# Performance work log

Measured on AMD Instinct MI355X. Metric: run time of the kernel, lower is better.

The kernel has to match this reference:

```python
import jax, jax.numpy as jnp
import numpy as np

B, L, C, NH = 4, 2048, 512, 8
HD = C // NH  # head_dim = 64


def setup_inputs() -> dict:
    key = jax.random.key(0)
    k1, k2, k3, k4 = jax.random.split(key, 4)
    s = 1.0 / np.sqrt(C)
    return {
        "x": jax.random.normal(k1, (B, L, C), dtype=jnp.float32),
        "w_qkv": jax.random.normal(k2, (C, 3 * C), dtype=jnp.float32) * s,
        "b_qkv": jnp.zeros((3 * C,), dtype=jnp.float32),  # zeroed in __init__
        "w_proj": jax.random.normal(k3, (C, C), dtype=jnp.float32) * s,
        "b_proj": jax.random.normal(k4, (C,), dtype=jnp.float32) * 0.01,
    }


def reference(x, w_qkv, b_qkv, w_proj, b_proj):
    Bx, Lx, Cx = x.shape
    qkv = x @ w_qkv + b_qkv                       # [B, L, 3C]
    qkv = qkv.reshape(Bx, Lx, 3, NH, HD)          # 'B L (K H D)'
    qkv = jnp.transpose(qkv, (2, 0, 3, 1, 4))     # 'K B H L D'
    q, k, v = qkv[0], qkv[1], qkv[2]
    scale = 1.0 / np.sqrt(HD)
    scores = jnp.einsum('bhld,bhmd->bhlm', q, k) * scale  # [B, H, L, L]
    attn = jax.nn.softmax(scores, axis=-1)
    out = jnp.einsum('bhlm,bhmd->bhld', attn, v)  # [B, H, L, D]
    out = jnp.transpose(out, (0, 2, 1, 3)).reshape(Bx, Lx, Cx)  # 'B H L D -> B L (H D)'
    return out @ w_proj + b_proj
```

## Files before the change

### kernel.cpp

```cpp
#include <hip/hip_runtime.h>

#define B_   4
#define L_   2048
#define C_   512
#define NH_  8
#define HD_  64
#define M_   (B_ * L_)
#define N_QKV 1536

typedef __bf16 bf16x8 __attribute__((ext_vector_type(8)));
typedef float floatx4 __attribute__((ext_vector_type(4)));
typedef unsigned short ushort_t;

__device__ __forceinline__ unsigned pk2(float a, float b) {
  union { float f; unsigned u; } x, y;
  x.f = a; y.f = b;
  return __builtin_amdgcn_perm(y.u + 0x8000u, x.u + 0x8000u, 0x07060302u);
}

__device__ __forceinline__ ushort_t bf16h(float a) {
  union { float f; unsigned u; } x;
  x.f = a;
  return (ushort_t)((x.u + 0x8000u) >> 16);
}

__device__ __forceinline__ floatx4 mfma16(bf16x8 a, bf16x8 b, floatx4 c) {
  return __builtin_amdgcn_mfma_f32_16x16x32_bf16(a, b, c, 0, 0, 0);
}

__device__ __forceinline__ void gld_lds16(const void* g, void* s) {
  __builtin_amdgcn_global_load_lds(
      (const __attribute__((address_space(1))) unsigned int*)(g),
      (__attribute__((address_space(3))) unsigned int*)(s), 16, 0, 0);
}

__global__ __launch_bounds__(256) void convert_all_kernel(
    const float* __restrict__ x, const float* __restrict__ wq,
    const float* __restrict__ wp, ushort_t* __restrict__ xb,
    ushort_t* __restrict__ wqT, ushort_t* __restrict__ wpT) {
  __shared__ ushort_t tile[64][68];
  const int t = threadIdx.x;
  const int bid = blockIdx.x;
  if (bid < 2048) {
    size_t i = ((size_t)bid * 256 + t) * 8;
    float4 a = *(const float4*)(x + i);
    float4 b = *(const float4*)(x + i + 4);
    uint4 o;
    o.x = pk2(a.x, a.y);
    o.y = pk2(a.z, a.w);
    o.z = pk2(b.x, b.y);
    o.w = pk2(b.z, b.w);
    *(uint4*)(xb + i) = o;
    return;
  }
  const float* w;
  ushort_t* wt;
  int N, n0, k0;
  if (bid < 2240) {
    int b2 = bid - 2048;
    w = wq; wt = wqT; N = N_QKV;
    n0 = (b2 % 24) * 64; k0 = (b2 / 24) * 64;
  } else {
    int b2 = bid - 2240;
    w = wp; wt = wpT; N = C_;
    n0 = (b2 & 7) * 64; k0 = (b2 >> 3) * 64;
  }
  const int r = t >> 4, c4 = (t & 15) * 4;
#pragma unroll
  for (int i = 0; i < 4; ++i) {
    int k = r + i * 16;
    float4 v = *(const float4*)(w + (size_t)(k0 + k) * N + n0 + c4);
    uint2 p;
    p.x = pk2(v.x, v.y);
    p.y = pk2(v.z, v.w);
    *(uint2*)&tile[k][c4] = p;
  }
  __syncthreads();
#pragma unroll
  for (int i = 0; i < 4; ++i) {
    int n = r + i * 16;
    uint2 o;
    o.x = (unsigned)tile[c4 + 0][n] | ((unsigned)tile[c4 + 1][n] << 16);
    o.y = (unsigned)tile[c4 + 2][n] | ((unsigned)tile[c4 + 3][n] << 16);
    *(uint2*)(wt + (size_t)(n0 + n) * 512 + k0 + c4) = o;
  }
}

__global__ __launch_bounds__(256) void qkv_mfma_kernel(
    const ushort_t* __restrict__ A,
    const ushort_t* __restrict__ Bt,
    const float* __restrict__ bias,
    ushort_t* __restrict__ Qd, ushort_t* __restrict__ Kd,
    ushort_t* __restrict__ Vd) {
  __shared__ ushort_t As[2][4096];
  __shared__ ushort_t Bs[2][2048];

  const int t = threadIdx.x;
  const int w = t >> 6, l = t & 63;
  const int li = l & 15, lq = l >> 4;
  const int m0 = blockIdx.x * 128;
  const int n0 = blockIdx.y * 64;

  const int inner = (l & 7) ^ (l >> 3);
  const int srow = (l >> 3) * 2 + (inner >> 2);
  const int skb = inner & 3;

  const ushort_t* asrc0 = A + (size_t)(m0 + (2 * w) * 16 + srow) * 512 + skb * 8;
  const ushort_t* asrc1 = A + (size_t)(m0 + (2 * w + 1) * 16 + srow) * 512 + skb * 8;
  const ushort_t* bsrc0 = Bt + (size_t)(n0 + w * 16 + srow) * 512 + skb * 8;
  const int qo0 = (2 * w) * 512, qo1 = (2 * w + 1) * 512;
  const int bo0 = w * 512;

  const int foff = (li >> 1) * 128 + ((((li & 1) * 4 + lq)) ^ (li >> 1)) * 16;

  const floatx4 fz = {0.f, 0.f, 0.f, 0.f};
  floatx4 acc[2][4];
#pragma unroll
  for (int i = 0; i < 2; ++i)
#pragma unroll
    for (int j = 0; j < 4; ++j) acc[i][j] = fz;

  for (int kk = 0; kk < 8; ++kk) {
    __syncthreads();
#pragma unroll
    for (int kh = 0; kh < 2; ++kh) {
      gld_lds16(asrc0 + kh * 32, &As[kh][qo0]);
      gld_lds16(asrc1 + kh * 32, &As[kh][qo1]);
      gld_lds16(bsrc0 + kh * 32, &Bs[kh][bo0]);
    }
    asrc0 += 64; asrc1 += 64; bsrc0 += 64;
    __syncthreads();

#pragma unroll
    for (int kh = 0; kh < 2; ++kh) {
      bf16x8 af[2], bfr[4];
#pragma unroll
      for (int mt = 0; mt < 2; ++mt)
        af[mt] = *(const bf16x8*)((const char*)&As[kh][0] +
                                  (w * 32 + mt * 16) * 64 + foff);
#pragma unroll
      for (int nt = 0; nt < 4; ++nt)
        bfr[nt] = *(const bf16x8*)((const char*)&Bs[kh][0] +
                                   (nt * 16) * 64 + foff);
#pragma unroll
      for (int mt = 0; mt < 2; ++mt)
#pragma unroll
        for (int nt = 0; nt < 4; ++nt)
          acc[mt][nt] = mfma16(af[mt], bfr[nt], acc[mt][nt]);
    }
  }

  const int kk2 = n0 >> 9, h = (n0 >> 6) & 7;
  const int mb = m0 + w * 32;
  const int b = m0 >> 11;
  const int bh = b * NH_ + h;
  const float SCQ = 0.18033688011f;
  float bb[4];
#pragma unroll
  for (int nt = 0; nt < 4; ++nt) bb[nt] = bias[n0 + nt * 16 + li];

  if (kk2 == 0) {
#pragma unroll
    for (int mt = 0; mt < 2; ++mt) {
      int lrow = (mb + mt * 16 + lq * 4) & (L_ - 1);
#pragma unroll
      for (int nt = 0; nt < 4; ++nt) {
        int d = nt * 16 + li;
        ushort_t* p = Qd + ((size_t)bh * L_ + lrow) * HD_ + d;
#pragma unroll
        for (int r = 0; r < 4; ++r)
          p[(size_t)r * HD_] = bf16h((acc[mt][nt][r] + bb[nt]) * SCQ);
      }
    }
  } else if (kk2 == 1) {
#pragma unroll
    for (int mt = 0; mt < 2; ++mt) {
      int lrow = (mb + mt * 16 + lq * 4) & (L_ - 1);
#pragma unroll
      for (int nt = 0; nt < 4; ++nt) {
        int d = nt * 16 + li;
        ushort_t* p = Kd + ((size_t)bh * L_ + lrow) * HD_ + d;
#pragma unroll
        for (int r = 0; r < 4; ++r)
          p[(size_t)r * HD_] = bf16h(acc[mt][nt][r] + bb[nt]);
      }
    }
  } else {
#pragma unroll
    for (int mt = 0; mt < 2; ++mt) {
      int tb = mb + mt * 16 + lq * 4;
      int key = tb & 63;
      int c = (tb >> 6) & 31;
      int sp = key >> 5;
      int rem = key & 31;
      int lq2 = rem >> 3;
      int h8 = (rem >> 2) & 1;
#pragma unroll
      for (int nt = 0; nt < 4; ++nt) {
        size_t off = ((size_t)(bh * 32 + c) * 512 +
                      ((sp * 4 + nt) * 4 + lq2) * 16 + li) * 8 + h8 * 4;
        uint2 v;
        v.x = pk2(acc[mt][nt][0] + bb[nt], acc[mt][nt][1] + bb[nt]);
        v.y = pk2(acc[mt][nt][2] + bb[nt], acc[mt][nt][3] + bb[nt]);
        *(uint2*)(Vd + off) = v;
      }
    }
  }
}

__global__ __launch_bounds__(512) void attn_kernel(
    const ushort_t* __restrict__ Qg, const ushort_t* __restrict__ Kg,
    const ushort_t* __restrict__ Vb, ushort_t* __restrict__ AO) {
  __shared__ __align__(16) char smem[35328];
  ushort_t* KsB = (ushort_t*)smem;
  ushort_t* VsB = (ushort_t*)(smem + 16384);
  float* Oc = (float*)smem;
  float* Lc = (float*)(smem + 34816);

  const int t = threadIdx.x;
  const int w = t >> 6, l = t & 63;
  const int g2 = w >> 2, wl = w & 3;
  const int li = l & 15, lq = l >> 4;
  const int bh = blockIdx.x & 31;
  const int m0 = (blockIdx.x >> 5) * 128;

  ushort_t* Ks = KsB + g2 * 4096;
  ushort_t* Vs = VsB + g2 * 4096;

  const ushort_t* ksrc[2];
  const ushort_t* vsrc[2];
  int koff[2];
#pragma unroll
  for (int u = 0; u < 2; ++u) {
    int p = (2 * wl + u) * 64 + l;
    int key = p >> 3, pb = p & 7;
    int swz = (key & 3) | (((key >> 3) & 1) << 2);
    ksrc[u] = Kg + ((size_t)bh * L_ + g2 * 1024 + key) * HD_ + (pb ^ swz) * 8;
    vsrc[u] = Vb + ((size_t)bh * 32 * 512 + (size_t)g2 * 16 * 512 + p) * 8;
    koff[u] = p * 8;
  }

  bf16x8 qf[2][2];
#pragma unroll
  for (int g = 0; g < 2; ++g)
#pragma unroll
    for (int s = 0; s < 2; ++s)
      qf[g][s] = *(const bf16x8*)(Qg +
          ((size_t)bh * L_ + m0 + wl * 32 + 16 * g + li) * HD_ + 32 * s + lq * 8);

  const floatx4 fz = {0.f, 0.f, 0.f, 0.f};
  floatx4 O[2][4];
  float lsum[2] = {0.f, 0.f};
#pragma unroll
  for (int g = 0; g < 2; ++g)
#pragma unroll
    for (int dt = 0; dt < 4; ++dt) O[g][dt] = fz;

  const int keybase = 8 * (li >> 2) + (li & 3);
  const int xsw = li & 7;

  for (int c = 0; c < 16; ++c) {
    __syncthreads();
#pragma unroll
    for (int u = 0; u < 2; ++u) {
      gld_lds16(ksrc[u], Ks + koff[u]);
      gld_lds16(vsrc[u], Vs + koff[u]);
      ksrc[u] += 64 * HD_;
      vsrc[u] += 4096;
    }
    __syncthreads();

#pragma unroll
    for (int sp = 0; sp < 2; ++sp) {
      floatx4 sa[2][2];
#pragma unroll
      for (int g = 0; g < 2; ++g)
#pragma unroll
        for (int k2 = 0; k2 < 2; ++k2) sa[g][k2] = fz;

#pragma unroll
      for (int k2 = 0; k2 < 2; ++k2) {
        const char* rowb =
            (const char*)Ks + (32 * sp + 4 * k2 + keybase) * 128;
#pragma unroll
        for (int s = 0; s < 2; ++s) {
          bf16x8 kf = *(const bf16x8*)(rowb + ((4 * s + lq) ^ xsw) * 16);
          sa[0][k2] = mfma16(kf, qf[0][s], sa[0][k2]);
          sa[1][k2] = mfma16(kf, qf[1][s], sa[1][k2]);
        }
      }

      bf16x8 pf[2];
#pragma unroll
      for (int g = 0; g < 2; ++g) {
        float pv[2][4];
#pragma unroll
        for (int k2 = 0; k2 < 2; ++k2)
#pragma unroll
          for (int r = 0; r < 4; ++r) {
            float e = __builtin_amdgcn_exp2f(sa[g][k2][r]);
            pv[k2][r] = e;
            lsum[g] += e;
          }
        uint4 pk;
        pk.x = pk2(pv[0][0], pv[0][1]);
        pk.y = pk2(pv[0][2], pv[0][3]);
        pk.z = pk2(pv[1][0], pv[1][1]);
        pk.w = pk2(pv[1][2], pv[1][3]);
        pf[g] = __builtin_bit_cast(bf16x8, pk);
      }

#pragma unroll
      for (int dt = 0; dt < 4; ++dt) {
        bf16x8 vf = *(const bf16x8*)((const char*)Vs +
            sp * 4096 + dt * 1024 + lq * 256 + li * 16);
        O[0][dt] = mfma16(vf, pf[0], O[0][dt]);
        O[1][dt] = mfma16(vf, pf[1], O[1][dt]);
      }
    }
  }

  float srow[2];
#pragma unroll
  for (int g = 0; g < 2; ++g) {
    float s = lsum[g];
    s += __shfl_xor(s, 16, 64);
    s += __shfl_xor(s, 32, 64);
    srow[g] = s;
  }

  __syncthreads();
  if (g2 == 1) {
#pragma unroll
    for (int g = 0; g < 2; ++g) {
      int row = wl * 32 + 16 * g + li;
#pragma unroll
      for (int dt = 0; dt < 4; ++dt)
        *(floatx4*)&Oc[row * 68 + 16 * dt + 4 * lq] = O[g][dt];
      Lc[row] = srow[g];
    }
  }
  __syncthreads();

  if (g2 == 0) {
    const int b = bh >> 3, h = bh & 7;
#pragma unroll
    for (int g = 0; g < 2; ++g) {
      int row = wl * 32 + 16 * g + li;
      float inv = 1.0f / (srow[g] + Lc[row]);
      int qrow = m0 + row;
      ushort_t* base = AO + ((size_t)(b * L_ + qrow)) * C_ + h * HD_ + 4 * lq;
#pragma unroll
      for (int dt = 0; dt < 4; ++dt) {
        floatx4 oc = *(const floatx4*)&Oc[row * 68 + 16 * dt + 4 * lq];
        floatx4 ot = O[g][dt] + oc;
        uint2 v;
        v.x = pk2(ot[0] * inv, ot[1] * inv);
        v.y = pk2(ot[2] * inv, ot[3] * inv);
        *(uint2*)(base + 16 * dt) = v;
      }
    }
  }
}

__global__ __launch_bounds__(256) void proj_mfma_kernel(
    const ushort_t* __restrict__ A,
    const ushort_t* __restrict__ Bt,
    const float* __restrict__ bias, float* __restrict__ out) {
  __shared__ ushort_t As[2][2048];
  __shared__ ushort_t Bs[2][2048];

  const int t = threadIdx.x;
  const int w = t >> 6, l = t & 63;
  const int li = l & 15, lq = l >> 4;
  const int m0 = blockIdx.x * 64;
  const int n0 = blockIdx.y * 64;

  const int inner = (l & 7) ^ (l >> 3);
  const int srow = (l >> 3) * 2 + (inner >> 2);
  const int skb = inner & 3;

  const ushort_t* asrc0 = A + (size_t)(m0 + w * 16 + srow) * 512 + skb * 8;
  const ushort_t* bsrc0 = Bt + (size_t)(n0 + w * 16 + srow) * 512 + skb * 8;
  const int qo0 = w * 512;

  const int foff = (li >> 1) * 128 + ((((li & 1) * 4 + lq)) ^ (li >> 1)) * 16;

  const floatx4 fz = {0.f, 0.f, 0.f, 0.f};
  floatx4 acc[4];
#pragma unroll
  for (int j = 0; j < 4; ++j) acc[j] = fz;

  for (int kk = 0; kk < 8; ++kk) {
    __syncthreads();
#pragma unroll
    for (int kh = 0; kh < 2; ++kh) {
      gld_lds16(asrc0 + kh * 32, &As[kh][qo0]);
      gld_lds16(bsrc0 + kh * 32, &Bs[kh][qo0]);
    }
    asrc0 += 64; bsrc0 += 64;
    __syncthreads();

#pragma unroll
    for (int kh = 0; kh < 2; ++kh) {
      bf16x8 af, bfr[4];
      af = *(const bf16x8*)((const char*)&As[kh][0] + (w * 16) * 64 + foff);
#pragma unroll
      for (int nt = 0; nt < 4; ++nt)
        bfr[nt] = *(const bf16x8*)((const char*)&Bs[kh][0] +
                                   (nt * 16) * 64 + foff);
#pragma unroll
      for (int nt = 0; nt < 4; ++nt)
        acc[nt] = mfma16(af, bfr[nt], acc[nt]);
    }
  }

  const int m = m0 + w * 16 + lq * 4;
#pragma unroll
  for (int nt = 0; nt < 4; ++nt) {
    int n = n0 + nt * 16 + li;
    float bb = bias[n];
#pragma unroll
    for (int r = 0; r < 4; ++r)
      out[(size_t)(m + r) * C_ + n] = acc[nt][r] + bb;
  }
}

extern "C" void kernel_launch(void* const* d_in, const int* in_sizes, int n_in,
                              void* d_out, int out_size, void* d_ws,
                              size_t ws_size, hipStream_t stream) {
  const float* x      = (const float*)d_in[0];
  const float* w_qkv  = (const float*)d_in[1];
  const float* b_qkv  = (const float*)d_in[2];
  const float* w_proj = (const float*)d_in[3];
  const float* b_proj = (const float*)d_in[4];
  float* out = (float*)d_out;

  ushort_t* ws     = (ushort_t*)d_ws;
  ushort_t* Qd     = ws;
  ushort_t* Kd     = ws + 4194304;
  ushort_t* Vd     = ws + 8388608;
  ushort_t* AO     = ws + 12582912;
  ushort_t* xb     = ws + 16777216;
  ushort_t* wqkvT  = ws + 20971520;
  ushort_t* wprojT = ws + 21757952;

  convert_all_kernel<<<2304, 256, 0, stream>>>(x, w_qkv, w_proj, xb, wqkvT,
                                               wprojT);

  dim3 g1(M_ / 128, N_QKV / 64);
  qkv_mfma_kernel<<<g1, 256, 0, stream>>>(xb, wqkvT, b_qkv, Qd, Kd, Vd);

  attn_kernel<<<512, 512, 0, stream>>>(Qd, Kd, Vd, AO);

  dim3 g3(M_ / 64, C_ / 64);
  proj_mfma_kernel<<<g3, 256, 0, stream>>>(AO, wprojT, b_proj, out);
}
```

Baseline: 148.5 us.

## Enlarge QKV GEMM tile to 128x128 and remap blocks per XCD

The QKV GEMM block tile grows from 128x64 to 128x128, with a 2x2 wave layout in which each wave computes a 64x64 sub-tile. This raises operand reuse from shared memory and halves the number of blocks. Both GEMMs now launch on a 1D grid whose block index is remapped so each XCD gets a contiguous band of M rows, aiming for better L2 locality of shared A/B tiles. The larger tile doubles accumulator registers and LDS use, which may lower occupancy. The V scatter index math is also rewritten to match the new per-wave row layout.

```diff
diff --git a/kernel.cpp b/kernel.cpp
--- a/kernel.cpp
+++ b/kernel.cpp
@@ -93,13 +93,16 @@
     ushort_t* __restrict__ Qd, ushort_t* __restrict__ Kd,
     ushort_t* __restrict__ Vd) {
   __shared__ ushort_t As[2][4096];
-  __shared__ ushort_t Bs[2][2048];
+  __shared__ ushort_t Bs[2][4096];
 
   const int t = threadIdx.x;
   const int w = t >> 6, l = t & 63;
   const int li = l & 15, lq = l >> 4;
-  const int m0 = blockIdx.x * 128;
-  const int n0 = blockIdx.y * 64;
+  const int wm = w & 1, wn = w >> 1;
+  const int bid = blockIdx.x;
+  const int xcd = bid & 7, idx = bid >> 3;
+  const int m0 = (xcd * 8 + idx / 12) * 128;
+  const int n0 = (idx % 12) * 128;
 
   const int inner = (l & 7) ^ (l >> 3);
   const int srow = (l >> 3) * 2 + (inner >> 2);
@@ -107,16 +110,16 @@
 
   const ushort_t* asrc0 = A + (size_t)(m0 + (2 * w) * 16 + srow) * 512 + skb * 8;
   const ushort_t* asrc1 = A + (size_t)(m0 + (2 * w + 1) * 16 + srow) * 512 + skb * 8;
-  const ushort_t* bsrc0 = Bt + (size_t)(n0 + w * 16 + srow) * 512 + skb * 8;
+  const ushort_t* bsrc0 = Bt + (size_t)(n0 + (2 * w) * 16 + srow) * 512 + skb * 8;
+  const ushort_t* bsrc1 = Bt + (size_t)(n0 + (2 * w + 1) * 16 + srow) * 512 + skb * 8;
   const int qo0 = (2 * w) * 512, qo1 = (2 * w + 1) * 512;
-  const int bo0 = w * 512;
 
   const int foff = (li >> 1) * 128 + ((((li & 1) * 4 + lq)) ^ (li >> 1)) * 16;
 
   const floatx4 fz = {0.f, 0.f, 0.f, 0.f};
-  floatx4 acc[2][4];
-#pragma unroll
-  for (int i = 0; i < 2; ++i)
+  floatx4 acc[4][4];
+#pragma unroll
+  for (int i = 0; i < 4; ++i)
 #pragma unroll
     for (int j = 0; j < 4; ++j) acc[i][j] = fz;
 
@@ -126,42 +129,44 @@
     for (int kh = 0; kh < 2; ++kh) {
       gld_lds16(asrc0 + kh * 32, &As[kh][qo0]);
       gld_lds16(asrc1 + kh * 32, &As[kh][qo1]);
-      gld_lds16(bsrc0 + kh * 32, &Bs[kh][bo0]);
-    }
-    asrc0 += 64; asrc1 += 64; bsrc0 += 64;
+      gld_lds16(bsrc0 + kh * 32, &Bs[kh][qo0]);
+      gld_lds16(bsrc1 + kh * 32, &Bs[kh][qo1]);
+    }
+    asrc0 += 64; asrc1 += 64; bsrc0 += 64; bsrc1 += 64;
     __syncthreads();
 
 #pragma unroll
     for (int kh = 0; kh < 2; ++kh) {
-      bf16x8 af[2], bfr[4];
-#pragma unroll
-      for (int mt = 0; mt < 2; ++mt)
+      bf16x8 af[4], bfr[4];
+#pragma unroll
+      for (int mt = 0; mt < 4; ++mt)
         af[mt] = *(const bf16x8*)((const char*)&As[kh][0] +
-                                  (w * 32 + mt * 16) * 64 + foff);
+                                  (wm * 64 + mt * 16) * 64 + foff);
 #pragma unroll
       for (int nt = 0; nt < 4; ++nt)
         bfr[nt] = *(const bf16x8*)((const char*)&Bs[kh][0] +
-                                   (nt * 16) * 64 + foff);
-#pragma unroll
-      for (int mt = 0; mt < 2; ++mt)
+                                   (wn * 64 + nt * 16) * 64 + foff);
+#pragma unroll
+      for (int mt = 0; mt < 4; ++mt)
 #pragma unroll
         for (int nt = 0; nt < 4; ++nt)
           acc[mt][nt] = mfma16(af[mt], bfr[nt], acc[mt][nt]);
     }
   }
 
-  const int kk2 = n0 >> 9, h = (n0 >> 6) & 7;
-  const int mb = m0 + w * 32;
-  const int b = m0 >> 11;
+  const int n0g = n0 + wn * 64;
+  const int kk2 = n0g >> 9, h = (n0g >> 6) & 7;
+  const int mb = m0 + wm * 64;
+  const int b = mb >> 11;
   const int bh = b * NH_ + h;
   const float SCQ = 0.18033688011f;
   float bb[4];
 #pragma unroll
-  for (int nt = 0; nt < 4; ++nt) bb[nt] = bias[n0 + nt * 16 + li];
+  for (int nt = 0; nt < 4; ++nt) bb[nt] = bias[n0g + nt * 16 + li];
 
   if (kk2 == 0) {
 #pragma unroll
-    for (int mt = 0; mt < 2; ++mt) {
+    for (int mt = 0; mt < 4; ++mt) {
       int lrow = (mb + mt * 16 + lq * 4) & (L_ - 1);
 #pragma unroll
       for (int nt = 0; nt < 4; ++nt) {
@@ -174,7 +179,7 @@
     }
   } else if (kk2 == 1) {
 #pragma unroll
-    for (int mt = 0; mt < 2; ++mt) {
+    for (int mt = 0; mt < 4; ++mt) {
       int lrow = (mb + mt * 16 + lq * 4) & (L_ - 1);
 #pragma unroll
       for (int nt = 0; nt < 4; ++nt) {
@@ -187,12 +192,11 @@
     }
   } else {
 #pragma unroll
-    for (int mt = 0; mt < 2; ++mt) {
+    for (int mt = 0; mt < 4; ++mt) {
       int tb = mb + mt * 16 + lq * 4;
-      int key = tb & 63;
       int c = (tb >> 6) & 31;
-      int sp = key >> 5;
-      int rem = key & 31;
+      int sp = (mt >> 1) & 1;
+      int rem = tb & 31;
       int lq2 = rem >> 3;
       int h8 = (rem >> 2) & 1;
 #pragma unroll
@@ -373,8 +377,10 @@
   const int t = threadIdx.x;
   const int w = t >> 6, l = t & 63;
   const int li = l & 15, lq = l >> 4;
-  const int m0 = blockIdx.x * 64;
-  const int n0 = blockIdx.y * 64;
+  const int bid = blockIdx.x;
+  const int xcd = bid & 7, idx = bid >> 3;
+  const int m0 = (xcd * 16 + (idx >> 3)) * 64;
+  const int n0 = (idx & 7) * 64;
 
   const int inner = (l & 7) ^ (l >> 3);
   const int srow = (l >> 3) * 2 + (inner >> 2);
@@ -448,11 +454,9 @@
   convert_all_kernel<<<2304, 256, 0, stream>>>(x, w_qkv, w_proj, xb, wqkvT,
                                                wprojT);
 
-  dim3 g1(M_ / 128, N_QKV / 64);
-  qkv_mfma_kernel<<<g1, 256, 0, stream>>>(xb, wqkvT, b_qkv, Qd, Kd, Vd);
+  qkv_mfma_kernel<<<768, 256, 0, stream>>>(xb, wqkvT, b_qkv, Qd, Kd, Vd);
 
   attn_kernel<<<512, 512, 0, stream>>>(Qd, Kd, Vd, AO);
 
-  dim3 g3(M_ / 64, C_ / 64);
-  proj_mfma_kernel<<<g3, 256, 0, stream>>>(AO, wprojT, b_proj, out);
-}
+  proj_mfma_kernel<<<1024, 256, 0, stream>>>(AO, wprojT, b_proj, out);
+}
```

After: 153.0 us. 3.0% more time.

## Split attention KV across four wave groups and remap GEMM blocks per XCD

Applied to the files above, without the earlier changes.

The attention kernel now handles 64 query rows per block with four wave-pairs, each covering a quarter of the keys. The partial outputs are merged through shared memory in three serialized steps, and the grid doubles to 1024 blocks. The QKV and projection GEMMs use a 1D grid remapped so that consecutive M tiles land on the same XCD, which should improve L2 reuse. In exchange, each block loads less per step and the serial reduction adds synchronization overhead.

```diff
diff --git a/kernel.cpp b/kernel.cpp
--- a/kernel.cpp
+++ b/kernel.cpp
@@ -98,8 +98,10 @@
   const int t = threadIdx.x;
   const int w = t >> 6, l = t & 63;
   const int li = l & 15, lq = l >> 4;
-  const int m0 = blockIdx.x * 128;
-  const int n0 = blockIdx.y * 64;
+  const int bid = blockIdx.x;
+  const int xcd = bid & 7, idx = bid >> 3;
+  const int m0 = (xcd * 8 + idx / 24) * 128;
+  const int n0 = (idx % 24) * 64;
 
   const int inner = (l & 7) ^ (l >> 3);
   const int srow = (l >> 3) * 2 + (inner >> 2);
@@ -208,35 +210,33 @@
   }
 }
 
-__global__ __launch_bounds__(512) void attn_kernel(
+__global__ __launch_bounds__(512, 8) void attn_kernel(
     const ushort_t* __restrict__ Qg, const ushort_t* __restrict__ Kg,
     const ushort_t* __restrict__ Vb, ushort_t* __restrict__ AO) {
-  __shared__ __align__(16) char smem[35328];
-  ushort_t* KsB = (ushort_t*)smem;
-  ushort_t* VsB = (ushort_t*)(smem + 16384);
-  float* Oc = (float*)smem;
-  float* Lc = (float*)(smem + 34816);
+  __shared__ __align__(16) char smem[32768];
 
   const int t = threadIdx.x;
   const int w = t >> 6, l = t & 63;
-  const int g2 = w >> 2, wl = w & 3;
+  const int g2 = w >> 1, wl = w & 1;
   const int li = l & 15, lq = l >> 4;
   const int bh = blockIdx.x & 31;
-  const int m0 = (blockIdx.x >> 5) * 128;
-
-  ushort_t* Ks = KsB + g2 * 4096;
-  ushort_t* Vs = VsB + g2 * 4096;
+  const int m0 = (blockIdx.x >> 5) * 64;
+
+  ushort_t* Ks = (ushort_t*)(smem + g2 * 4096);
+  ushort_t* Vs = (ushort_t*)(smem + 16384 + g2 * 4096);
+  float* Oc = (float*)smem;
+  float* Lc = (float*)(smem + 17408);
 
   const ushort_t* ksrc[2];
   const ushort_t* vsrc[2];
   int koff[2];
 #pragma unroll
   for (int u = 0; u < 2; ++u) {
-    int p = (2 * wl + u) * 64 + l;
+    int p = wl * 128 + u * 64 + l;
     int key = p >> 3, pb = p & 7;
     int swz = (key & 3) | (((key >> 3) & 1) << 2);
-    ksrc[u] = Kg + ((size_t)bh * L_ + g2 * 1024 + key) * HD_ + (pb ^ swz) * 8;
-    vsrc[u] = Vb + ((size_t)bh * 32 * 512 + (size_t)g2 * 16 * 512 + p) * 8;
+    ksrc[u] = Kg + ((size_t)bh * L_ + g2 * 512 + key) * HD_ + (pb ^ swz) * 8;
+    vsrc[u] = Vb + ((size_t)(bh * 32 + g2 * 8) * 512 + p) * 8;
     koff[u] = p * 8;
   }
 
@@ -265,58 +265,54 @@
     for (int u = 0; u < 2; ++u) {
       gld_lds16(ksrc[u], Ks + koff[u]);
       gld_lds16(vsrc[u], Vs + koff[u]);
-      ksrc[u] += 64 * HD_;
-      vsrc[u] += 4096;
-    }
-    __syncthreads();
-
-#pragma unroll
-    for (int sp = 0; sp < 2; ++sp) {
-      floatx4 sa[2][2];
-#pragma unroll
-      for (int g = 0; g < 2; ++g)
-#pragma unroll
-        for (int k2 = 0; k2 < 2; ++k2) sa[g][k2] = fz;
-
-#pragma unroll
-      for (int k2 = 0; k2 < 2; ++k2) {
-        const char* rowb =
-            (const char*)Ks + (32 * sp + 4 * k2 + keybase) * 128;
-#pragma unroll
-        for (int s = 0; s < 2; ++s) {
-          bf16x8 kf = *(const bf16x8*)(rowb + ((4 * s + lq) ^ xsw) * 16);
-          sa[0][k2] = mfma16(kf, qf[0][s], sa[0][k2]);
-          sa[1][k2] = mfma16(kf, qf[1][s], sa[1][k2]);
+      ksrc[u] += 32 * HD_;
+      vsrc[u] += 2048;
+    }
+    __syncthreads();
+
+    floatx4 sa[2][2];
+#pragma unroll
+    for (int g = 0; g < 2; ++g)
+#pragma unroll
+      for (int k2 = 0; k2 < 2; ++k2) sa[g][k2] = fz;
+
+#pragma unroll
+    for (int k2 = 0; k2 < 2; ++k2) {
+      const char* rowb = (const char*)Ks + (4 * k2 + keybase) * 128;
+#pragma unroll
+      for (int s = 0; s < 2; ++s) {
+        bf16x8 kf = *(const bf16x8*)(rowb + ((4 * s + lq) ^ xsw) * 16);
+        sa[0][k2] = mfma16(kf, qf[0][s], sa[0][k2]);
+        sa[1][k2] = mfma16(kf, qf[1][s], sa[1][k2]);
+      }
+    }
+
+    bf16x8 pf[2];
+#pragma unroll
+    for (int g = 0; g < 2; ++g) {
+      float pv[2][4];
+#pragma unroll
+      for (int k2 = 0; k2 < 2; ++k2)
+#pragma unroll
+        for (int r = 0; r < 4; ++r) {
+          float e = __builtin_amdgcn_exp2f(sa[g][k2][r]);
+          pv[k2][r] = e;
+          lsum[g] += e;
         }
-      }
-
-      bf16x8 pf[2];
-#pragma unroll
-      for (int g = 0; g < 2; ++g) {
-        float pv[2][4];
-#pragma unroll
-        for (int k2 = 0; k2 < 2; ++k2)
-#pragma unroll
-          for (int r = 0; r < 4; ++r) {
-            float e = __builtin_amdgcn_exp2f(sa[g][k2][r]);
-            pv[k2][r] = e;
-            lsum[g] += e;
-          }
-        uint4 pk;
-        pk.x = pk2(pv[0][0], pv[0][1]);
-        pk.y = pk2(pv[0][2], pv[0][3]);
-        pk.z = pk2(pv[1][0], pv[1][1]);
-        pk.w = pk2(pv[1][2], pv[1][3]);
-        pf[g] = __builtin_bit_cast(bf16x8, pk);
-      }
-
-#pragma unroll
-      for (int dt = 0; dt < 4; ++dt) {
-        bf16x8 vf = *(const bf16x8*)((const char*)Vs +
-            sp * 4096 + dt * 1024 + lq * 256 + li * 16);
-        O[0][dt] = mfma16(vf, pf[0], O[0][dt]);
-        O[1][dt] = mfma16(vf, pf[1], O[1][dt]);
-      }
+      uint4 pk;
+      pk.x = pk2(pv[0][0], pv[0][1]);
+      pk.y = pk2(pv[0][2], pv[0][3]);
+      pk.z = pk2(pv[1][0], pv[1][1]);
+      pk.w = pk2(pv[1][2], pv[1][3]);
+      pf[g] = __builtin_bit_cast(bf16x8, pk);
+    }
+
+#pragma unroll
+    for (int dt = 0; dt < 4; ++dt) {
+      bf16x8 vf = *(const bf16x8*)((const char*)Vs +
+          dt * 1024 + lq * 256 + li * 16);
+      O[0][dt] = mfma16(vf, pf[0], O[0][dt]);
+      O[1][dt] = mfma16(vf, pf[1], O[1][dt]);
     }
   }
 
@@ -330,18 +326,43 @@
   }
 
   __syncthreads();
-  if (g2 == 1) {
+  if (g2 == 3) {
 #pragma unroll
     for (int g = 0; g < 2; ++g) {
       int row = wl * 32 + 16 * g + li;
 #pragma unroll
       for (int dt = 0; dt < 4; ++dt)
         *(floatx4*)&Oc[row * 68 + 16 * dt + 4 * lq] = O[g][dt];
-      Lc[row] = srow[g];
+      if (lq == 0) Lc[row] = srow[g];
     }
   }
   __syncthreads();
-
+  if (g2 == 2) {
+#pragma unroll
+    for (int g = 0; g < 2; ++g) {
+      int row = wl * 32 + 16 * g + li;
+#pragma unroll
+      for (int dt = 0; dt < 4; ++dt) {
+        floatx4 oc = *(const floatx4*)&Oc[row * 68 + 16 * dt + 4 * lq];
+        *(floatx4*)&Oc[row * 68 + 16 * dt + 4 * lq] = oc + O[g][dt];
+      }
+      if (lq == 0) Lc[row] += srow[g];
+    }
+  }
+  __syncthreads();
+  if (g2 == 1) {
+#pragma unroll
+    for (int g = 0; g < 2; ++g) {
+      int row = wl * 32 + 16 * g + li;
+#pragma unroll
+      for (int dt = 0; dt < 4; ++dt) {
+        floatx4 oc = *(const floatx4*)&Oc[row * 68 + 16 * dt + 4 * lq];
+        *(floatx4*)&Oc[row * 68 + 16 * dt + 4 * lq] = oc + O[g][dt];
+      }
+      if (lq == 0) Lc[row] += srow[g];
+    }
+  }
+  __syncthreads();
   if (g2 == 0) {
     const int b = bh >> 3, h = bh & 7;
 #pragma unroll
@@ -373,8 +394,10 @@
   const int t = threadIdx.x;
   const int w = t >> 6, l = t & 63;
   const int li = l & 15, lq = l >> 4;
-  const int m0 = blockIdx.x * 64;
-  const int n0 = blockIdx.y * 64;
+  const int bid = blockIdx.x;
+  const int xcd = bid & 7, idx = bid >> 3;
+  const int m0 = (xcd * 16 + (idx >> 3)) * 64;
+  const int n0 = (idx & 7) * 64;
 
   const int inner = (l & 7) ^ (l >> 3);
   const int srow = (l >> 3) * 2 + (inner >> 2);
@@ -448,11 +471,9 @@
   convert_all_kernel<<<2304, 256, 0, stream>>>(x, w_qkv, w_proj, xb, wqkvT,
                                                wprojT);
 
-  dim3 g1(M_ / 128, N_QKV / 64);
-  qkv_mfma_kernel<<<g1, 256, 0, stream>>>(xb, wqkvT, b_qkv, Qd, Kd, Vd);
-
-  attn_kernel<<<512, 512, 0, stream>>>(Qd, Kd, Vd, AO);
-
-  dim3 g3(M_ / 64, C_ / 64);
-  proj_mfma_kernel<<<g3, 256, 0, stream>>>(AO, wprojT, b_proj, out);
-}
+  qkv_mfma_kernel<<<1536, 256, 0, stream>>>(xb, wqkvT, b_qkv, Qd, Kd, Vd);
+
+  attn_kernel<<<1024, 512, 0, stream>>>(Qd, Kd, Vd, AO);
+
+  proj_mfma_kernel<<<1024, 256, 0, stream>>>(AO, wprojT, b_proj, out);
+}
```

Result: slower. 335.5 us (+125.9%).

## Fuse x fp32-to-bf16 conversion into QKV GEMM tile loads

Applied to the files above, without the earlier changes.

Drops the standalone pass that converted x to bf16 and instead has the QKV GEMM load fp32 x directly, pack it to bf16 in registers and store it into shared memory. This removes one kernel launch and the write and re-read of a bf16 copy of x. In exchange, each GEMM column tile re-reads x at twice the byte width, and the A-tile load becomes a synchronous register round trip instead of an asynchronous direct-to-LDS load.

```diff
diff --git a/kernel.cpp b/kernel.cpp
--- a/kernel.cpp
+++ b/kernel.cpp
@@ -34,34 +34,20 @@
       (__attribute__((address_space(3))) unsigned int*)(s), 16, 0, 0);
 }
 
-__global__ __launch_bounds__(256) void convert_all_kernel(
-    const float* __restrict__ x, const float* __restrict__ wq,
-    const float* __restrict__ wp, ushort_t* __restrict__ xb,
+__global__ __launch_bounds__(256) void convert_w_kernel(
+    const float* __restrict__ wq, const float* __restrict__ wp,
     ushort_t* __restrict__ wqT, ushort_t* __restrict__ wpT) {
   __shared__ ushort_t tile[64][68];
   const int t = threadIdx.x;
   const int bid = blockIdx.x;
-  if (bid < 2048) {
-    size_t i = ((size_t)bid * 256 + t) * 8;
-    float4 a = *(const float4*)(x + i);
-    float4 b = *(const float4*)(x + i + 4);
-    uint4 o;
-    o.x = pk2(a.x, a.y);
-    o.y = pk2(a.z, a.w);
-    o.z = pk2(b.x, b.y);
-    o.w = pk2(b.z, b.w);
-    *(uint4*)(xb + i) = o;
-    return;
-  }
   const float* w;
   ushort_t* wt;
   int N, n0, k0;
-  if (bid < 2240) {
-    int b2 = bid - 2048;
+  if (bid < 192) {
     w = wq; wt = wqT; N = N_QKV;
-    n0 = (b2 % 24) * 64; k0 = (b2 / 24) * 64;
+    n0 = (bid % 24) * 64; k0 = (bid / 24) * 64;
   } else {
-    int b2 = bid - 2240;
+    int b2 = bid - 192;
     w = wp; wt = wpT; N = C_;
     n0 = (b2 & 7) * 64; k0 = (b2 >> 3) * 64;
   }
@@ -87,7 +73,7 @@
 }
 
 __global__ __launch_bounds__(256) void qkv_mfma_kernel(
-    const ushort_t* __restrict__ A,
+    const float* __restrict__ X,
     const ushort_t* __restrict__ Bt,
     const float* __restrict__ bias,
     ushort_t* __restrict__ Qd, ushort_t* __restrict__ Kd,
@@ -105,11 +91,12 @@
   const int srow = (l >> 3) * 2 + (inner >> 2);
   const int skb = inner & 3;
 
-  const ushort_t* asrc0 = A + (size_t)(m0 + (2 * w) * 16 + srow) * 512 + skb * 8;
-  const ushort_t* asrc1 = A + (size_t)(m0 + (2 * w + 1) * 16 + srow) * 512 + skb * 8;
+  const float* axsrc0 = X + (size_t)(m0 + (2 * w) * 16 + srow) * 512 + skb * 8;
+  const float* axsrc1 = X + (size_t)(m0 + (2 * w + 1) * 16 + srow) * 512 + skb * 8;
   const ushort_t* bsrc0 = Bt + (size_t)(n0 + w * 16 + srow) * 512 + skb * 8;
-  const int qo0 = (2 * w) * 512, qo1 = (2 * w + 1) * 512;
   const int bo0 = w * 512;
+  const int ao0 = (2 * w) * 512 + l * 8;
+  const int ao1 = (2 * w + 1) * 512 + l * 8;
 
   const int foff = (li >> 1) * 128 + ((((li & 1) * 4 + lq)) ^ (li >> 1)) * 16;
 
@@ -121,14 +108,31 @@
     for (int j = 0; j < 4; ++j) acc[i][j] = fz;
 
   for (int kk = 0; kk < 8; ++kk) {
-    __syncthreads();
-#pragma unroll
-    for (int kh = 0; kh < 2; ++kh) {
-      gld_lds16(asrc0 + kh * 32, &As[kh][qo0]);
-      gld_lds16(asrc1 + kh * 32, &As[kh][qo1]);
-      gld_lds16(bsrc0 + kh * 32, &Bs[kh][bo0]);
-    }
-    asrc0 += 64; asrc1 += 64; bsrc0 += 64;
+    float4 av[2][2][2];
+#pragma unroll
+    for (int u = 0; u < 2; ++u)
+#pragma unroll
+      for (int kh = 0; kh < 2; ++kh) {
+        const float* s = (u ? axsrc1 : axsrc0) + kh * 32;
+        av[u][kh][0] = *(const float4*)s;
+        av[u][kh][1] = *(const float4*)(s + 4);
+      }
+    axsrc0 += 64; axsrc1 += 64;
+    __syncthreads();
+    gld_lds16(bsrc0, &Bs[0][bo0]);
+    gld_lds16(bsrc0 + 32, &Bs[1][bo0]);
+    bsrc0 += 64;
+#pragma unroll
+    for (int u = 0; u < 2; ++u)
+#pragma unroll
+      for (int kh = 0; kh < 2; ++kh) {
+        uint4 o;
+        o.x = pk2(av[u][kh][0].x, av[u][kh][0].y);
+        o.y = pk2(av[u][kh][0].z, av[u][kh][0].w);
+        o.z = pk2(av[u][kh][1].x, av[u][kh][1].y);
+        o.w = pk2(av[u][kh][1].z, av[u][kh][1].w);
+        *(uint4*)&As[kh][u ? ao1 : ao0] = o;
+      }
     __syncthreads();
 
 #pragma unroll
@@ -441,15 +445,13 @@
   ushort_t* Kd     = ws + 4194304;
   ushort_t* Vd     = ws + 8388608;
   ushort_t* AO     = ws + 12582912;
-  ushort_t* xb     = ws + 16777216;
-  ushort_t* wqkvT  = ws + 20971520;
-  ushort_t* wprojT = ws + 21757952;
-
-  convert_all_kernel<<<2304, 256, 0, stream>>>(x, w_qkv, w_proj, xb, wqkvT,
-                                               wprojT);
+  ushort_t* wqkvT  = ws + 16777216;
+  ushort_t* wprojT = ws + 17563648;
+
+  convert_w_kernel<<<256, 256, 0, stream>>>(w_qkv, w_proj, wqkvT, wprojT);
 
   dim3 g1(M_ / 128, N_QKV / 64);
-  qkv_mfma_kernel<<<g1, 256, 0, stream>>>(xb, wqkvT, b_qkv, Qd, Kd, Vd);
+  qkv_mfma_kernel<<<g1, 256, 0, stream>>>(x, wqkvT, b_qkv, Qd, Kd, Vd);
 
   attn_kernel<<<512, 512, 0, stream>>>(Qd, Kd, Vd, AO);
 
```

Measured after the change: 152.5 us. +2.7%, slower.
